# Optimization experiments

Hardware: AMD Instinct MI355X
Metric: run time of the kernel (lower is better)

Reference implementation:

```python
import jax, jax.numpy as jnp
import numpy as np

B, SQ, SKV, D = 4, 2048, 2048, 1024
HEADS, DIM_HEAD = 16, 64
SCALE = DIM_HEAD ** -0.5


def setup_inputs() -> dict:
    key = jax.random.key(0)
    ks = jax.random.split(key, 7)
    s = 0.02  # keep pre-softmax logits in a sane range
    return {
        "hidden_states": jax.random.normal(ks[0], (B, SQ, D), dtype=jnp.float32),
        "encoder_hidden_states": jax.random.normal(ks[1], (B, SKV, D), dtype=jnp.float32),
        "Wq": jax.random.normal(ks[2], (D, D), dtype=jnp.float32) * s,
        "Wk": jax.random.normal(ks[3], (D, D), dtype=jnp.float32) * s,
        "Wv": jax.random.normal(ks[4], (D, D), dtype=jnp.float32) * s,
        "Wo": jax.random.normal(ks[5], (D, D), dtype=jnp.float32) * s,
        "bo": jnp.zeros((D,), dtype=jnp.float32),
    }


def reference(hidden_states, encoder_hidden_states, Wq, Wk, Wv, Wo, bo):
    # to_q / to_k / to_v (bias=False)
    q = hidden_states @ Wq                       # [B, SQ, H*Dh]
    k = encoder_hidden_states @ Wk               # [B, SKV, H*Dh]
    v = encoder_hidden_states @ Wv
    # head split: [B, S, H, Dh]
    q = q.reshape(B, SQ, HEADS, DIM_HEAD)
    k = k.reshape(B, SKV, HEADS, DIM_HEAD)
    v = v.reshape(B, SKV, HEADS, DIM_HEAD)
    # scaled QK^T (baddbmm with beta=0, alpha=scale), softmax over keys
    scores = jnp.einsum("bqhd,bkhd->bhqk", q, k) * SCALE  # [B, H, SQ, SKV]
    probs = jax.nn.softmax(scores, axis=-1)
    # attention-weighted values, merge heads
    out = jnp.einsum("bhqk,bkhd->bqhd", probs, v).reshape(B, SQ, HEADS * DIM_HEAD)
    # to_out[0] linear (with bias); to_out[1] Dropout(0.0) is identity
    return out @ Wo + bo
```

## Files before the change

kernel.cpp:

```cpp
#include <hip/hip_runtime.h>

#define BATCH 4
#define SQ 2048
#define SKV 2048
#define DMODEL 1024
#define HEADS 16
#define DH 64

typedef __bf16 bf8_t __attribute__((ext_vector_type(8)));
typedef float f4_t __attribute__((ext_vector_type(4)));
typedef float f16_t __attribute__((ext_vector_type(16)));
typedef unsigned int u32;

static __device__ __forceinline__ unsigned short f2bf(float f) {
  __bf16 h = (__bf16)f;
  return __builtin_bit_cast(unsigned short, h);
}
static __device__ __forceinline__ u32 pk2(float a, float b) {
  return (u32)f2bf(a) | ((u32)f2bf(b) << 16);
}
static __device__ __forceinline__ void async16(const unsigned short* g, unsigned short* l) {
  __builtin_amdgcn_global_load_lds((const __attribute__((address_space(1))) unsigned int*)g,
                                   (__attribute__((address_space(3))) unsigned int*)l, 16, 0, 0);
}

__global__ __launch_bounds__(256) void wtrans_k(const float* __restrict__ W0,
                                                const float* __restrict__ W1,
                                                const float* __restrict__ W2,
                                                const float* __restrict__ W3,
                                                unsigned short* __restrict__ out) {
  __shared__ unsigned short t[64][72];
  const float* W = blockIdx.z == 0 ? W0 : blockIdx.z == 1 ? W1 : blockIdx.z == 2 ? W2 : W3;
  const float scl = (blockIdx.z == 0) ? 0.125f * 1.44269504088896f : 1.0f;
  unsigned short* o = out + (size_t)blockIdx.z * (DMODEL * DMODEL);
  const int tid = threadIdx.x;
  const int k0 = blockIdx.x * 64, n0 = blockIdx.y * 64;
#pragma unroll
  for (int it = 0; it < 4; ++it) {
    int c = tid + it * 256;
    int r = c >> 4, q4 = c & 15;
    float4 v = *reinterpret_cast<const float4*>(&W[(size_t)(k0 + r) * DMODEL + n0 + q4 * 4]);
    t[q4 * 4 + 0][r] = f2bf(v.x * scl);
    t[q4 * 4 + 1][r] = f2bf(v.y * scl);
    t[q4 * 4 + 2][r] = f2bf(v.z * scl);
    t[q4 * 4 + 3][r] = f2bf(v.w * scl);
  }
  __syncthreads();
#pragma unroll
  for (int it = 0; it < 2; ++it) {
    int c = tid + it * 256;
    int r = c >> 3, s8 = c & 7;
    uint4 pv;
    pv.x = (u32)t[r][s8 * 8 + 0] | ((u32)t[r][s8 * 8 + 1] << 16);
    pv.y = (u32)t[r][s8 * 8 + 2] | ((u32)t[r][s8 * 8 + 3] << 16);
    pv.z = (u32)t[r][s8 * 8 + 4] | ((u32)t[r][s8 * 8 + 5] << 16);
    pv.w = (u32)t[r][s8 * 8 + 6] | ((u32)t[r][s8 * 8 + 7] << 16);
    *reinterpret_cast<uint4*>(&o[(size_t)(n0 + r) * DMODEL + k0 + s8 * 8]) = pv;
  }
}

template <int MODE>
__global__ __launch_bounds__(256, 2) void gemm_k(const void* __restrict__ Ap,
                                                 const unsigned short* __restrict__ BT,
                                                 void* __restrict__ Cp,
                                                 const float* __restrict__ bias) {
  __shared__ unsigned short As[128 * 64];
  __shared__ unsigned short Bs[128 * 64];
  const int tid = threadIdx.x;
  const int lane = tid & 63, w = tid >> 6;
  const int wr = w >> 1, wc = w & 1;
  const int lr = lane & 15, lg = lane >> 4;
  const int m0 = blockIdx.x * 128, n0 = blockIdx.y * 128;
  f4_t acc[4][4] = {};
  for (int kt = 0; kt < DMODEL / 64; ++kt) {
    const int kb = kt * 64;
#pragma unroll
    for (int ch = 0; ch < 4; ++ch) {
      const int c = tid + ch * 256;
      const int m = c >> 3, k8 = c & 7;
      const int idx = (m * 64 + k8 * 8) ^ ((m & 7) << 3);
      if constexpr (MODE == 3) {
        uint4 v = *reinterpret_cast<const uint4*>((const unsigned short*)Ap +
                                                  (size_t)(m0 + m) * DMODEL + kb + k8 * 8);
        *reinterpret_cast<uint4*>(&As[idx]) = v;
      } else {
        const float* src = (const float*)Ap + (size_t)(m0 + m) * DMODEL + kb + k8 * 8;
        float4 v0 = *reinterpret_cast<const float4*>(src);
        float4 v1 = *reinterpret_cast<const float4*>(src + 4);
        uint4 u;
        u.x = pk2(v0.x, v0.y);
        u.y = pk2(v0.z, v0.w);
        u.z = pk2(v1.x, v1.y);
        u.w = pk2(v1.z, v1.w);
        *reinterpret_cast<uint4*>(&As[idx]) = u;
      }
      uint4 bv = *reinterpret_cast<const uint4*>(&BT[(size_t)(n0 + m) * DMODEL + kb + k8 * 8]);
      *reinterpret_cast<uint4*>(&Bs[idx]) = bv;
    }
    __syncthreads();
#pragma unroll
    for (int ks = 0; ks < 2; ++ks) {
      bf8_t a[4], b[4];
#pragma unroll
      for (int rf = 0; rf < 4; ++rf) {
        const int row = wr * 64 + rf * 16 + lr;
        a[rf] = *reinterpret_cast<const bf8_t*>(
            &As[(row * 64 + ks * 32 + lg * 8) ^ ((row & 7) << 3)]);
      }
#pragma unroll
      for (int cf = 0; cf < 4; ++cf) {
        const int nn = wc * 64 + cf * 16 + lr;
        b[cf] = *reinterpret_cast<const bf8_t*>(
            &Bs[(nn * 64 + ks * 32 + lg * 8) ^ ((nn & 7) << 3)]);
      }
#pragma unroll
      for (int rf = 0; rf < 4; ++rf)
#pragma unroll
        for (int cf = 0; cf < 4; ++cf)
          acc[rf][cf] = __builtin_amdgcn_mfma_f32_16x16x32_bf16(a[rf], b[cf], acc[rf][cf], 0, 0, 0);
    }
    __syncthreads();
  }
  if constexpr (MODE == 0) {
    unsigned short* C = (unsigned short*)Cp;
#pragma unroll
    for (int rf = 0; rf < 4; ++rf)
#pragma unroll
      for (int cf = 0; cf < 4; ++cf)
#pragma unroll
        for (int i = 0; i < 4; ++i) {
          const int row = m0 + wr * 64 + rf * 16 + lg * 4 + i;
          const int col = n0 + wc * 64 + cf * 16 + lr;
          C[(size_t)row * DMODEL + col] = f2bf(acc[rf][cf][i]);
        }
  } else if constexpr (MODE == 2) {
    unsigned short* VTp = (unsigned short*)Cp;
#pragma unroll
    for (int rf = 0; rf < 4; ++rf)
#pragma unroll
      for (int cf = 0; cf < 4; ++cf) {
        const int row0 = m0 + wr * 64 + rf * 16 + lg * 4;
        const int bb = row0 >> 11, s0 = row0 & 2047;
        const int n = n0 + wc * 64 + cf * 16 + lr;
        ushort4 u;
        u.x = f2bf(acc[rf][cf][0]);
        u.y = f2bf(acc[rf][cf][1]);
        u.z = f2bf(acc[rf][cf][2]);
        u.w = f2bf(acc[rf][cf][3]);
        *reinterpret_cast<ushort4*>(&VTp[(size_t)(bb * 1024 + n) * SKV + s0]) = u;
      }
  } else {
    float* C = (float*)Cp;
#pragma unroll
    for (int cf = 0; cf < 4; ++cf) {
      const int col = n0 + wc * 64 + cf * 16 + lr;
      const float bv = bias[col];
#pragma unroll
      for (int rf = 0; rf < 4; ++rf)
#pragma unroll
        for (int i = 0; i < 4; ++i) {
          const int row = m0 + wr * 64 + rf * 16 + lg * 4 + i;
          C[(size_t)row * DMODEL + col] = acc[rf][cf][i] + bv;
        }
    }
  }
}

__global__ __launch_bounds__(256, 4) void attn_k(const unsigned short* __restrict__ Qb,
                                                 const unsigned short* __restrict__ Kb,
                                                 const unsigned short* __restrict__ VT,
                                                 unsigned short* __restrict__ AO) {
  __shared__ unsigned short Ks[2][64 * 64];
  __shared__ unsigned short Vs[2][64 * 64];
  const int tid = threadIdx.x;
  const int lane = tid & 63, w = tid >> 6;
  const int rw = lane & 31, hi = lane >> 5;

  const int bid = blockIdx.x;
  const int swz = (bid & 7) * 128 + (bid >> 3);
  const int hl = swz >> 4;
  const int qb = swz & 15;
  const int b = hl >> 4, h = hl & 15;
  const int q0 = qb * 128 + w * 32;

  const unsigned short* Qp = Qb + ((size_t)(b * SQ + q0 + rw)) * DMODEL + h * DH + hi * 8;
  bf8_t qf[4];
#pragma unroll
  for (int f = 0; f < 4; ++f)
    qf[f] = *reinterpret_cast<const bf8_t*>(Qp + 16 * f);

  f16_t acc0 = {}, acc1 = {};
  float mrow = -1e30f, lsum = 0.f;

  const unsigned short* Kh = Kb + (size_t)(b * SKV) * DMODEL + h * DH;
  const unsigned short* Vh = VT + (size_t)(b * 1024 + h * DH) * SKV;

  auto stage = [&](int bf, int kt) {
    const int kv0 = kt * 64;
#pragma unroll
    for (int ch = 0; ch < 2; ++ch) {
      const int g = ch * 256 + tid;
      const int r = g >> 3, s8 = (g & 7) ^ (r & 7);
      unsigned short* kdst = &Ks[bf][(ch * 256 + w * 64) * 8];
      unsigned short* vdst = &Vs[bf][(ch * 256 + w * 64) * 8];
      async16(Kh + (size_t)(kv0 + r) * DMODEL + s8 * 8, kdst);
      async16(Vh + (size_t)r * SKV + kv0 + s8 * 8, vdst);
    }
  };

  stage(0, 0);
  __syncthreads();

  int cur = 0;
  for (int kt = 0; kt < SKV / 64; ++kt) {
    if (kt + 1 < SKV / 64) stage(cur ^ 1, kt + 1);

    f16_t s0 = {}, s1 = {};
    __builtin_amdgcn_s_setprio(1);
#pragma unroll
    for (int f = 0; f < 4; ++f) {
      const int gcol = ((2 * f + hi) ^ (rw & 7)) * 8;
      bf8_t k0 = *reinterpret_cast<const bf8_t*>(&Ks[cur][rw * 64 + gcol]);
      bf8_t k1 = *reinterpret_cast<const bf8_t*>(&Ks[cur][(rw + 32) * 64 + gcol]);
      s0 = __builtin_amdgcn_mfma_f32_32x32x16_bf16(k0, qf[f], s0, 0, 0, 0);
      s1 = __builtin_amdgcn_mfma_f32_32x32x16_bf16(k1, qf[f], s1, 0, 0, 0);
    }
    __builtin_amdgcn_s_setprio(0);

    float pmax = -1e30f;
#pragma unroll
    for (int i = 0; i < 16; ++i) pmax = fmaxf(pmax, fmaxf(s0[i], s1[i]));
    pmax = fmaxf(pmax, __shfl_xor(pmax, 32, 64));
    if (__any(pmax > mrow + 8.f)) {
      const float mnew = fmaxf(mrow, pmax);
      const float scl = __builtin_amdgcn_exp2f(mrow - mnew);
      lsum *= scl;
#pragma unroll
      for (int i = 0; i < 16; ++i) {
        acc0[i] *= scl;
        acc1[i] *= scl;
      }
      mrow = mnew;
    }
    float sum = 0.f;
#pragma unroll
    for (int i = 0; i < 16; ++i) {
      s0[i] = __builtin_amdgcn_exp2f(s0[i] - mrow);
      sum += s0[i];
    }
#pragma unroll
    for (int i = 0; i < 16; ++i) {
      s1[i] = __builtin_amdgcn_exp2f(s1[i] - mrow);
      sum += s1[i];
    }
    lsum += sum;

    __builtin_amdgcn_s_setprio(1);
#pragma unroll
    for (int kb = 0; kb < 2; ++kb) {
      const f16_t& sv = kb ? s1 : s0;
      bf8_t pf[2];
      {
        u32 w0 = pk2(sv[0], sv[1]), w2 = pk2(sv[4], sv[5]);
        asm volatile("v_permlane32_swap_b32 %0, %1" : "+v"(w0), "+v"(w2));
        u32 w1 = pk2(sv[2], sv[3]), w3 = pk2(sv[6], sv[7]);
        asm volatile("v_permlane32_swap_b32 %0, %1" : "+v"(w1), "+v"(w3));
        uint4 t0 = {w0, w1, w2, w3};
        pf[0] = __builtin_bit_cast(bf8_t, t0);
        u32 x0 = pk2(sv[8], sv[9]), x2 = pk2(sv[12], sv[13]);
        asm volatile("v_permlane32_swap_b32 %0, %1" : "+v"(x0), "+v"(x2));
        u32 x1 = pk2(sv[10], sv[11]), x3 = pk2(sv[14], sv[15]);
        asm volatile("v_permlane32_swap_b32 %0, %1" : "+v"(x1), "+v"(x3));
        uint4 t1 = {x0, x1, x2, x3};
        pf[1] = __builtin_bit_cast(bf8_t, t1);
      }
#pragma unroll
      for (int s = 0; s < 2; ++s) {
        const int g = 4 * kb + 2 * s + hi;
        const int gcol = ((g ^ (rw & 7)) * 8);
        bf8_t v0 = *reinterpret_cast<const bf8_t*>(&Vs[cur][rw * 64 + gcol]);
        bf8_t v1 = *reinterpret_cast<const bf8_t*>(&Vs[cur][(rw + 32) * 64 + gcol]);
        acc0 = __builtin_amdgcn_mfma_f32_32x32x16_bf16(v0, pf[s], acc0, 0, 0, 0);
        acc1 = __builtin_amdgcn_mfma_f32_32x32x16_bf16(v1, pf[s], acc1, 0, 0, 0);
      }
    }
    __builtin_amdgcn_s_setprio(0);

    __syncthreads();
    cur ^= 1;
  }

  const float lrow = lsum + __shfl_xor(lsum, 32, 64);
  const float inv = 1.f / lrow;
  unsigned short* Op = AO + ((size_t)(b * SQ + q0 + rw)) * DMODEL + h * DH;
#pragma unroll
  for (int db = 0; db < 2; ++db) {
    const f16_t& A = db ? acc1 : acc0;
#pragma unroll
    for (int r = 0; r < 16; r += 2) {
      const int d = db * 32 + (r & 3) + 8 * (r >> 2) + 4 * hi;
      *reinterpret_cast<u32*>(Op + d) = pk2(A[r] * inv, A[r + 1] * inv);
    }
  }
}

extern "C" void kernel_launch(void* const* d_in, const int* in_sizes, int n_in,
                              void* d_out, int out_size, void* d_ws, size_t ws_size,
                              hipStream_t stream) {
  const float* hs = (const float*)d_in[0];
  const float* ehs = (const float*)d_in[1];
  const float* Wq = (const float*)d_in[2];
  const float* Wk = (const float*)d_in[3];
  const float* Wv = (const float*)d_in[4];
  const float* Wo = (const float*)d_in[5];
  const float* bo = (const float*)d_in[6];
  float* out = (float*)d_out;

  unsigned short* ws = (unsigned short*)d_ws;
  const size_t MM = (size_t)1024 * 1024;
  unsigned short* wT = ws;
  unsigned short* Qb = ws + 4 * MM;
  unsigned short* Kb = Qb + 8 * MM;
  unsigned short* VTb = Kb + 8 * MM;
  unsigned short* AO = VTb + 8 * MM;

  wtrans_k<<<dim3(16, 16, 4), 256, 0, stream>>>(Wq, Wk, Wv, Wo, wT);
  gemm_k<0><<<dim3(64, 8), 256, 0, stream>>>(hs, wT + 0 * MM, Qb, nullptr);
  gemm_k<0><<<dim3(64, 8), 256, 0, stream>>>(ehs, wT + 1 * MM, Kb, nullptr);
  gemm_k<2><<<dim3(64, 8), 256, 0, stream>>>(ehs, wT + 2 * MM, VTb, nullptr);
  attn_k<<<dim3(1024), 256, 0, stream>>>(Qb, Kb, VTb, AO);
  gemm_k<3><<<dim3(64, 8), 256, 0, stream>>>(AO, wT + 3 * MM, out, bo);
}
```

Baseline: 224.3 us.

## Pre-convert inputs to bf16, merge QKV GEMMs, double-buffer async GEMM loads

A new kernel converts hidden_states and encoder_hidden_states to bf16 up front, staging them in the output buffer as scratch. The three projection GEMMs are merged into one 1536-block launch. The GEMM kernel now double-buffers LDS tiles with async global-to-LDS loads and raises MFMA priority. It also bumps attention occupancy to 5 blocks per SM and uses max3 in the row-max. The aim is to cut launch count, remove per-tile fp32 conversion from the GEMM inner loop and overlap loads with compute, at the cost of doubled LDS per GEMM block and an extra conversion pass.

New measurement: 243.7 us. 1.09x slower.

```diff
diff --git a/kernel.cpp b/kernel.cpp
--- a/kernel.cpp
+++ b/kernel.cpp
@@ -11,28 +11,44 @@
 typedef float f4_t __attribute__((ext_vector_type(4)));
 typedef float f16_t __attribute__((ext_vector_type(16)));
 typedef unsigned int u32;
-
-static __device__ __forceinline__ unsigned short f2bf(float f) {
+typedef unsigned short ush;
+
+static __device__ __forceinline__ ush f2bf(float f) {
   __bf16 h = (__bf16)f;
-  return __builtin_bit_cast(unsigned short, h);
+  return __builtin_bit_cast(ush, h);
 }
 static __device__ __forceinline__ u32 pk2(float a, float b) {
   return (u32)f2bf(a) | ((u32)f2bf(b) << 16);
 }
-static __device__ __forceinline__ void async16(const unsigned short* g, unsigned short* l) {
+static __device__ __forceinline__ float max3f(float a, float b, float c) {
+  return fmaxf(fmaxf(a, b), c);
+}
+static __device__ __forceinline__ void async16(const ush* g, ush* l) {
   __builtin_amdgcn_global_load_lds((const __attribute__((address_space(1))) unsigned int*)g,
                                    (__attribute__((address_space(3))) unsigned int*)l, 16, 0, 0);
+}
+
+__global__ __launch_bounds__(256) void cvt_k(const float* __restrict__ X0,
+                                             const float* __restrict__ X1,
+                                             ush* __restrict__ Y0, ush* __restrict__ Y1) {
+  const float* X = blockIdx.y ? X1 : X0;
+  ush* Y = blockIdx.y ? Y1 : Y0;
+  const size_t i = ((size_t)blockIdx.x * 256 + threadIdx.x) * 8;
+  float4 a = *reinterpret_cast<const float4*>(X + i);
+  float4 b = *reinterpret_cast<const float4*>(X + i + 4);
+  uint4 u = {pk2(a.x, a.y), pk2(a.z, a.w), pk2(b.x, b.y), pk2(b.z, b.w)};
+  *reinterpret_cast<uint4*>(Y + i) = u;
 }
 
 __global__ __launch_bounds__(256) void wtrans_k(const float* __restrict__ W0,
                                                 const float* __restrict__ W1,
                                                 const float* __restrict__ W2,
                                                 const float* __restrict__ W3,
-                                                unsigned short* __restrict__ out) {
-  __shared__ unsigned short t[64][72];
+                                                ush* __restrict__ out) {
+  __shared__ ush t[64][72];
   const float* W = blockIdx.z == 0 ? W0 : blockIdx.z == 1 ? W1 : blockIdx.z == 2 ? W2 : W3;
   const float scl = (blockIdx.z == 0) ? 0.125f * 1.44269504088896f : 1.0f;
-  unsigned short* o = out + (size_t)blockIdx.z * (DMODEL * DMODEL);
+  ush* o = out + (size_t)blockIdx.z * (DMODEL * DMODEL);
   const int tid = threadIdx.x;
   const int k0 = blockIdx.x * 64, n0 = blockIdx.y * 64;
 #pragma unroll
@@ -59,45 +75,43 @@
   }
 }
 
-template <int MODE>
-__global__ __launch_bounds__(256, 2) void gemm_k(const void* __restrict__ Ap,
-                                                 const unsigned short* __restrict__ BT,
-                                                 void* __restrict__ Cp,
-                                                 const float* __restrict__ bias) {
-  __shared__ unsigned short As[128 * 64];
-  __shared__ unsigned short Bs[128 * 64];
+__global__ __launch_bounds__(256, 2) void proj_k(const ush* __restrict__ hsb,
+                                                 const ush* __restrict__ ehsb,
+                                                 const ush* __restrict__ AO,
+                                                 const ush* __restrict__ wT,
+                                                 ush* __restrict__ Qb, ush* __restrict__ Kb,
+                                                 ush* __restrict__ VTb, float* __restrict__ out,
+                                                 const float* __restrict__ bias, int segbase) {
+  __shared__ ush As[2][128 * 64];
+  __shared__ ush Bs[2][128 * 64];
   const int tid = threadIdx.x;
   const int lane = tid & 63, w = tid >> 6;
   const int wr = w >> 1, wc = w & 1;
   const int lr = lane & 15, lg = lane >> 4;
-  const int m0 = blockIdx.x * 128, n0 = blockIdx.y * 128;
+  const int bid = blockIdx.x;
+  const int seg = segbase + (bid >> 9);
+  const int t = bid & 511;
+  const int m0 = (t >> 3) * 128, n0 = (t & 7) * 128;
+  const ush* A = seg == 0 ? hsb : (seg == 3 ? AO : ehsb);
+  const ush* BT = wT + (size_t)seg * (DMODEL * DMODEL);
+
+  auto stage = [&](int bf, int kt) {
+    const int kb = kt * 64;
+#pragma unroll
+    for (int ch = 0; ch < 4; ++ch) {
+      const int g = ch * 256 + tid;
+      const int r = g >> 3, s8 = (g & 7) ^ (r & 7);
+      async16(A + (size_t)(m0 + r) * DMODEL + kb + s8 * 8, &As[bf][(ch * 256 + w * 64) * 8]);
+      async16(BT + (size_t)(n0 + r) * DMODEL + kb + s8 * 8, &Bs[bf][(ch * 256 + w * 64) * 8]);
+    }
+  };
+
   f4_t acc[4][4] = {};
+  stage(0, 0);
+  __syncthreads();
   for (int kt = 0; kt < DMODEL / 64; ++kt) {
-    const int kb = kt * 64;
-#pragma unroll
-    for (int ch = 0; ch < 4; ++ch) {
-      const int c = tid + ch * 256;
-      const int m = c >> 3, k8 = c & 7;
-      const int idx = (m * 64 + k8 * 8) ^ ((m & 7) << 3);
-      if constexpr (MODE == 3) {
-        uint4 v = *reinterpret_cast<const uint4*>((const unsigned short*)Ap +
-                                                  (size_t)(m0 + m) * DMODEL + kb + k8 * 8);
-        *reinterpret_cast<uint4*>(&As[idx]) = v;
-      } else {
-        const float* src = (const float*)Ap + (size_t)(m0 + m) * DMODEL + kb + k8 * 8;
-        float4 v0 = *reinterpret_cast<const float4*>(src);
-        float4 v1 = *reinterpret_cast<const float4*>(src + 4);
-        uint4 u;
-        u.x = pk2(v0.x, v0.y);
-        u.y = pk2(v0.z, v0.w);
-        u.z = pk2(v1.x, v1.y);
-        u.w = pk2(v1.z, v1.w);
-        *reinterpret_cast<uint4*>(&As[idx]) = u;
-      }
-      uint4 bv = *reinterpret_cast<const uint4*>(&BT[(size_t)(n0 + m) * DMODEL + kb + k8 * 8]);
-      *reinterpret_cast<uint4*>(&Bs[idx]) = bv;
-    }
-    __syncthreads();
+    const int cur = kt & 1;
+    if (kt + 1 < DMODEL / 64) stage(cur ^ 1, kt + 1);
 #pragma unroll
     for (int ks = 0; ks < 2; ++ks) {
       bf8_t a[4], b[4];
@@ -105,36 +119,25 @@
       for (int rf = 0; rf < 4; ++rf) {
         const int row = wr * 64 + rf * 16 + lr;
         a[rf] = *reinterpret_cast<const bf8_t*>(
-            &As[(row * 64 + ks * 32 + lg * 8) ^ ((row & 7) << 3)]);
+            &As[cur][(row * 64 + ks * 32 + lg * 8) ^ ((row & 7) << 3)]);
       }
 #pragma unroll
       for (int cf = 0; cf < 4; ++cf) {
         const int nn = wc * 64 + cf * 16 + lr;
         b[cf] = *reinterpret_cast<const bf8_t*>(
-            &Bs[(nn * 64 + ks * 32 + lg * 8) ^ ((nn & 7) << 3)]);
-      }
+            &Bs[cur][(nn * 64 + ks * 32 + lg * 8) ^ ((nn & 7) << 3)]);
+      }
+      __builtin_amdgcn_s_setprio(1);
 #pragma unroll
       for (int rf = 0; rf < 4; ++rf)
 #pragma unroll
         for (int cf = 0; cf < 4; ++cf)
           acc[rf][cf] = __builtin_amdgcn_mfma_f32_16x16x32_bf16(a[rf], b[cf], acc[rf][cf], 0, 0, 0);
+      __builtin_amdgcn_s_setprio(0);
     }
     __syncthreads();
   }
-  if constexpr (MODE == 0) {
-    unsigned short* C = (unsigned short*)Cp;
-#pragma unroll
-    for (int rf = 0; rf < 4; ++rf)
-#pragma unroll
-      for (int cf = 0; cf < 4; ++cf)
-#pragma unroll
-        for (int i = 0; i < 4; ++i) {
-          const int row = m0 + wr * 64 + rf * 16 + lg * 4 + i;
-          const int col = n0 + wc * 64 + cf * 16 + lr;
-          C[(size_t)row * DMODEL + col] = f2bf(acc[rf][cf][i]);
-        }
-  } else if constexpr (MODE == 2) {
-    unsigned short* VTp = (unsigned short*)Cp;
+  if (seg == 2) {
 #pragma unroll
     for (int rf = 0; rf < 4; ++rf)
 #pragma unroll
@@ -147,10 +150,9 @@
         u.y = f2bf(acc[rf][cf][1]);
         u.z = f2bf(acc[rf][cf][2]);
         u.w = f2bf(acc[rf][cf][3]);
-        *reinterpret_cast<ushort4*>(&VTp[(size_t)(bb * 1024 + n) * SKV + s0]) = u;
-      }
-  } else {
-    float* C = (float*)Cp;
+        *reinterpret_cast<ushort4*>(&VTb[(size_t)(bb * 1024 + n) * SKV + s0]) = u;
+      }
+  } else if (seg == 3) {
 #pragma unroll
     for (int cf = 0; cf < 4; ++cf) {
       const int col = n0 + wc * 64 + cf * 16 + lr;
@@ -160,18 +162,30 @@
 #pragma unroll
         for (int i = 0; i < 4; ++i) {
           const int row = m0 + wr * 64 + rf * 16 + lg * 4 + i;
-          C[(size_t)row * DMODEL + col] = acc[rf][cf][i] + bv;
+          out[(size_t)row * DMODEL + col] = acc[rf][cf][i] + bv;
         }
     }
-  }
-}
-
-__global__ __launch_bounds__(256, 4) void attn_k(const unsigned short* __restrict__ Qb,
-                                                 const unsigned short* __restrict__ Kb,
-                                                 const unsigned short* __restrict__ VT,
-                                                 unsigned short* __restrict__ AO) {
-  __shared__ unsigned short Ks[2][64 * 64];
-  __shared__ unsigned short Vs[2][64 * 64];
+  } else {
+    ush* C = seg == 0 ? Qb : Kb;
+#pragma unroll
+    for (int rf = 0; rf < 4; ++rf)
+#pragma unroll
+      for (int cf = 0; cf < 4; ++cf)
+#pragma unroll
+        for (int i = 0; i < 4; ++i) {
+          const int row = m0 + wr * 64 + rf * 16 + lg * 4 + i;
+          const int col = n0 + wc * 64 + cf * 16 + lr;
+          C[(size_t)row * DMODEL + col] = f2bf(acc[rf][cf][i]);
+        }
+  }
+}
+
+__global__ __launch_bounds__(256, 5) void attn_k(const ush* __restrict__ Qb,
+                                                 const ush* __restrict__ Kb,
+                                                 const ush* __restrict__ VT,
+                                                 ush* __restrict__ AO) {
+  __shared__ ush Ks[2][64 * 64];
+  __shared__ ush Vs[2][64 * 64];
   const int tid = threadIdx.x;
   const int lane = tid & 63, w = tid >> 6;
   const int rw = lane & 31, hi = lane >> 5;
@@ -183,17 +197,16 @@
   const int b = hl >> 4, h = hl & 15;
   const int q0 = qb * 128 + w * 32;
 
-  const unsigned short* Qp = Qb + ((size_t)(b * SQ + q0 + rw)) * DMODEL + h * DH + hi * 8;
+  const ush* Qp = Qb + ((size_t)(b * SQ + q0 + rw)) * DMODEL + h * DH + hi * 8;
   bf8_t qf[4];
 #pragma unroll
-  for (int f = 0; f < 4; ++f)
-    qf[f] = *reinterpret_cast<const bf8_t*>(Qp + 16 * f);
+  for (int f = 0; f < 4; ++f) qf[f] = *reinterpret_cast<const bf8_t*>(Qp + 16 * f);
 
   f16_t acc0 = {}, acc1 = {};
   float mrow = -1e30f, lsum = 0.f;
 
-  const unsigned short* Kh = Kb + (size_t)(b * SKV) * DMODEL + h * DH;
-  const unsigned short* Vh = VT + (size_t)(b * 1024 + h * DH) * SKV;
+  const ush* Kh = Kb + (size_t)(b * SKV) * DMODEL + h * DH;
+  const ush* Vh = VT + (size_t)(b * 1024 + h * DH) * SKV;
 
   auto stage = [&](int bf, int kt) {
     const int kv0 = kt * 64;
@@ -201,8 +214,8 @@
     for (int ch = 0; ch < 2; ++ch) {
       const int g = ch * 256 + tid;
       const int r = g >> 3, s8 = (g & 7) ^ (r & 7);
-      unsigned short* kdst = &Ks[bf][(ch * 256 + w * 64) * 8];
-      unsigned short* vdst = &Vs[bf][(ch * 256 + w * 64) * 8];
+      ush* kdst = &Ks[bf][(ch * 256 + w * 64) * 8];
+      ush* vdst = &Vs[bf][(ch * 256 + w * 64) * 8];
       async16(Kh + (size_t)(kv0 + r) * DMODEL + s8 * 8, kdst);
       async16(Vh + (size_t)r * SKV + kv0 + s8 * 8, vdst);
     }
@@ -227,9 +240,9 @@
     }
     __builtin_amdgcn_s_setprio(0);
 
-    float pmax = -1e30f;
-#pragma unroll
-    for (int i = 0; i < 16; ++i) pmax = fmaxf(pmax, fmaxf(s0[i], s1[i]));
+    float pmax = fmaxf(s0[0], s1[0]);
+#pragma unroll
+    for (int i = 1; i < 16; ++i) pmax = max3f(s0[i], s1[i], pmax);
     pmax = fmaxf(pmax, __shfl_xor(pmax, 32, 64));
     if (__any(pmax > mrow + 8.f)) {
       const float mnew = fmaxf(mrow, pmax);
@@ -292,7 +305,7 @@
 
   const float lrow = lsum + __shfl_xor(lsum, 32, 64);
   const float inv = 1.f / lrow;
-  unsigned short* Op = AO + ((size_t)(b * SQ + q0 + rw)) * DMODEL + h * DH;
+  ush* Op = AO + ((size_t)(b * SQ + q0 + rw)) * DMODEL + h * DH;
 #pragma unroll
   for (int db = 0; db < 2; ++db) {
     const f16_t& A = db ? acc1 : acc0;
@@ -313,8 +326,10 @@
   const float* Wk = (const float*)d_in[3];
   const float* Wv = (const float*)d_in[4];
   const float* Wo = (const float*)d_in[5];
+  const float* Wo_ = (const float*)d_in[5];
   const float* bo = (const float*)d_in[6];
   float* out = (float*)d_out;
+  (void)Wo_;
 
   unsigned short* ws = (unsigned short*)d_ws;
   const size_t MM = (size_t)1024 * 1024;
@@ -323,11 +338,12 @@
   unsigned short* Kb = Qb + 8 * MM;
   unsigned short* VTb = Kb + 8 * MM;
   unsigned short* AO = VTb + 8 * MM;
-
+  unsigned short* hsb = (unsigned short*)d_out;
+  unsigned short* ehsb = hsb + 8 * MM;
+
+  cvt_k<<<dim3(4096, 2), 256, 0, stream>>>(hs, ehs, hsb, ehsb);
   wtrans_k<<<dim3(16, 16, 4), 256, 0, stream>>>(Wq, Wk, Wv, Wo, wT);
-  gemm_k<0><<<dim3(64, 8), 256, 0, stream>>>(hs, wT + 0 * MM, Qb, nullptr);
-  gemm_k<0><<<dim3(64, 8), 256, 0, stream>>>(ehs, wT + 1 * MM, Kb, nullptr);
-  gemm_k<2><<<dim3(64, 8), 256, 0, stream>>>(ehs, wT + 2 * MM, VTb, nullptr);
+  proj_k<<<dim3(1536), 256, 0, stream>>>(hsb, ehsb, AO, wT, Qb, Kb, VTb, out, bo, 0);
   attn_k<<<dim3(1024), 256, 0, stream>>>(Qb, Kb, VTb, AO);
-  gemm_k<3><<<dim3(64, 8), 256, 0, stream>>>(AO, wT + 3 * MM, out, bo);
-}
+  proj_k<<<dim3(512), 256, 0, stream>>>(hsb, ehsb, AO, wT, Qb, Kb, VTb, out, bo, 3);
+}
```
